# Performance work log

Hardware: AMD Instinct MI355X
Metric: run time of the kernel (lower is better)

The kernel has to match this reference:

```python
import jax, jax.numpy as jnp
import numpy as np

B, T, D = 4096, 64, 250          # batch states, tokens, BiLSTM output size (2*hidden_dim)
S_STACK, S_BUF = 3, 1            # num_stack, num_buffer
H, N_TRANS, N_LABELS = 125, 4, 50


def setup_inputs() -> dict:
    key = jax.random.key(0)
    ks = jax.random.split(key, 16)
    inp = {
        "lstm_out":     jax.random.normal(ks[0], (B, T, D), jnp.float32),
        "stack_index":  jax.random.randint(ks[1], (B, S_STACK), 0, T),
        "stack_len":    jax.random.randint(ks[2], (B,), 0, S_STACK + 1),
        "buffer_index": jax.random.randint(ks[3], (B, S_BUF), 0, T),
        "buffer_len":   jax.random.randint(ks[4], (B,), 0, S_BUF + 1),
        "W1_t": jax.random.normal(ks[5], ((S_STACK + S_BUF) * D, H), jnp.float32) * 0.03,
        "b1_t": jax.random.normal(ks[6], (H,), jnp.float32) * 0.03,
        "W2_t": jax.random.normal(ks[7], (H, N_TRANS), jnp.float32) * 0.03,
        "b2_t": jax.random.normal(ks[8], (N_TRANS,), jnp.float32) * 0.03,
        "W1_r": jax.random.normal(ks[9], ((S_STACK + S_BUF) * D, H), jnp.float32) * 0.03,
        "b1_r": jax.random.normal(ks[10], (H,), jnp.float32) * 0.03,
        "W2_r": jax.random.normal(ks[11], (H, N_LABELS), jnp.float32) * 0.03,
        "b2_r": jax.random.normal(ks[12], (N_LABELS,), jnp.float32) * 0.03,
    }
    return inp


def _gather_pad(lstm_out, index, length):
    # lstm_out: [B, T, D]; index: [B, K]; length: [B]
    # positions >= length[b] receive the zero padding vector (== _mlp_padding)
    g = jnp.take_along_axis(lstm_out, index[:, :, None], axis=1)      # [B, K, D]
    mask = jnp.arange(index.shape[1])[None, :] < length[:, None]      # [B, K]
    g = jnp.where(mask[:, :, None], g, jnp.zeros((), g.dtype))
    return g.reshape(g.shape[0], -1)                                  # [B, K*D]


def _mlp(x, W1, b1, W2, b2):
    # MultilayerPerceptron(input, 125, out) with tanh hidden activation
    h = jnp.tanh(x @ W1 + b1)
    return h @ W2 + b2


def reference(lstm_out, stack_index, stack_len, buffer_index, buffer_len,
              W1_t, b1_t, W2_t, b2_t, W1_r, b1_r, W2_r, b2_r):
    stack_feats = _gather_pad(lstm_out, stack_index, stack_len)    # [B, 3*D]
    buf_feats = _gather_pad(lstm_out, buffer_index, buffer_len)    # [B, 1*D]
    mlp_input = jnp.concatenate([stack_feats, buf_feats], axis=1)  # [B, 4*D]
    # dropout is identity in eval mode
    transitions = jnp.tanh(_mlp(mlp_input, W1_t, b1_t, W2_t, b2_t))
    relations = jnp.tanh(_mlp(mlp_input, W1_r, b1_r, W2_r, b2_r))
    return transitions, relations
```

## Files before the change

### kernel.cpp

```cpp
#include <hip/hip_runtime.h>

#define BATCH 4096
#define TSEQ  64
#define DDIM  250
#define HDIM  125
#define NT    4
#define NL    50
#define KP    1024
#define NP    256

typedef __attribute__((ext_vector_type(8))) __bf16 bf16x8;
typedef __attribute__((ext_vector_type(4))) float  f32x4;

__device__ __forceinline__ unsigned short f32_to_bf16(float f) {
    unsigned int u = __float_as_uint(f);
    u += 0x7FFFu + ((u >> 16) & 1u);
    return (unsigned short)(u >> 16);
}

__global__ __launch_bounds__(256) void prep_kernel(
    const float* __restrict__ lstm_out,
    const int*   __restrict__ stack_index,
    const int*   __restrict__ stack_len,
    const int*   __restrict__ buffer_index,
    const int*   __restrict__ buffer_len,
    const float* __restrict__ W1_t,
    const float* __restrict__ W1_r,
    unsigned short* __restrict__ Xb,
    unsigned short* __restrict__ Wb)
{
    const int blk = blockIdx.x;
    const int t   = threadIdx.x;

    if (blk < BATCH) {
        const int b    = blk;
        const int slen = stack_len[b];
        const int blen = buffer_len[b];
        const int idxB = buffer_index[b];
        const int k0   = t * 4;
        unsigned short v[4];
        #pragma unroll
        for (int i = 0; i < 4; ++i) {
            const int k = k0 + i;
            float f = 0.0f;
            if (k < 1000) {
                const int s = k / 250;
                const int d = k - s * 250;
                const int idxS = stack_index[b * 3 + (s < 3 ? s : 2)];
                const int idx  = (s < 3) ? idxS : idxB;
                const bool valid = (s < 3) ? (s < slen) : (blen > 0);
                if (valid) f = lstm_out[((size_t)b * TSEQ + (size_t)idx) * DDIM + d];
            }
            v[i] = f32_to_bf16(f);
        }
        *reinterpret_cast<ushort4*>(Xb + (size_t)b * KP + k0) =
            make_ushort4(v[0], v[1], v[2], v[3]);
    } else {
        const int n  = blk - BATCH;
        const int k0 = t * 4;
        unsigned short v[4];
        #pragma unroll
        for (int i = 0; i < 4; ++i) {
            const int k = k0 + i;
            float f = 0.0f;
            if (k < 1000 && n < 250) {
                f = (n < HDIM) ? W1_t[(size_t)k * HDIM + n]
                               : W1_r[(size_t)k * HDIM + (n - HDIM)];
            }
            v[i] = f32_to_bf16(f);
        }
        *reinterpret_cast<ushort4*>(Wb + (size_t)n * KP + k0) =
            make_ushort4(v[0], v[1], v[2], v[3]);
    }
}

__global__ __launch_bounds__(256) void gemm_kernel(
    const unsigned short* __restrict__ Xb,
    const unsigned short* __restrict__ Wb,
    const float* __restrict__ b1_t,
    const float* __restrict__ b1_r,
    const float* __restrict__ W2_t,
    const float* __restrict__ b2_t,
    const float* __restrict__ W2_r,
    const float* __restrict__ b2_r,
    float* __restrict__ out_trans,
    float* __restrict__ out_rel)
{
    __shared__ __align__(16) unsigned char XsRaw[16 * 2048];
    __shared__ float h_lds[16][260];

    const int tid = threadIdx.x;
    const int b0  = blockIdx.x * 16;

    #pragma unroll
    for (int i = 0; i < 8; ++i) {
        const int chunk = i * 256 + tid;
        const int row   = chunk >> 7;
        const int c     = chunk & 127;
        uint4 g = *reinterpret_cast<const uint4*>(Xb + (size_t)(b0 + row) * KP + c * 8);
        const int byte = row * 2048 + ((c * 16) ^ ((row & 7) << 4));
        *reinterpret_cast<uint4*>(XsRaw + byte) = g;
    }
    __syncthreads();

    const int lane  = tid & 63;
    const int wave  = tid >> 6;
    const int lrow  = lane & 15;
    const int lk    = (lane >> 4) * 8;
    const int nbase = wave * 64;

    f32x4 acc0 = {0.f,0.f,0.f,0.f}, acc1 = acc0, acc2 = acc0, acc3 = acc0;

    const unsigned short* wbase = Wb + (size_t)(nbase + lrow) * KP + lk;
    const unsigned char*  xrow  = XsRaw + lrow * 2048;
    const int xmask = (lrow & 7) << 4;

    #pragma unroll 8
    for (int ks = 0; ks < 32; ++ks) {
        const int xbyte = ((ks * 32 + lk) * 2) ^ xmask;
        bf16x8 a   = *reinterpret_cast<const bf16x8*>(xrow + xbyte);
        bf16x8 bv0 = *reinterpret_cast<const bf16x8*>(wbase + 0 * 16 * KP + ks * 32);
        bf16x8 bv1 = *reinterpret_cast<const bf16x8*>(wbase + 1 * 16 * KP + ks * 32);
        bf16x8 bv2 = *reinterpret_cast<const bf16x8*>(wbase + 2 * 16 * KP + ks * 32);
        bf16x8 bv3 = *reinterpret_cast<const bf16x8*>(wbase + 3 * 16 * KP + ks * 32);
        acc0 = __builtin_amdgcn_mfma_f32_16x16x32_bf16(a, bv0, acc0, 0, 0, 0);
        acc1 = __builtin_amdgcn_mfma_f32_16x16x32_bf16(a, bv1, acc1, 0, 0, 0);
        acc2 = __builtin_amdgcn_mfma_f32_16x16x32_bf16(a, bv2, acc2, 0, 0, 0);
        acc3 = __builtin_amdgcn_mfma_f32_16x16x32_bf16(a, bv3, acc3, 0, 0, 0);
    }

    {
        const int r0 = (lane >> 4) * 4;
        #pragma unroll
        for (int fn = 0; fn < 4; ++fn) {
            const f32x4 ac = (fn == 0) ? acc0 : (fn == 1) ? acc1 : (fn == 2) ? acc2 : acc3;
            const int col = nbase + fn * 16 + lrow;
            const float bias = (col < HDIM) ? b1_t[col]
                             : (col < 250)  ? b1_r[col - HDIM] : 0.0f;
            #pragma unroll
            for (int rg = 0; rg < 4; ++rg) {
                const float v = tanhf(ac[rg] + bias);
                if (col < HDIM)      h_lds[r0 + rg][col] = v;
                else if (col < 250)  h_lds[r0 + rg][col + 3] = v;
            }
        }
    }
    __syncthreads();

    const int m  = tid & 15;
    const int og = tid >> 4;
    if (og < 14) {
        const bool isT = (og == 0);
        const int  base = isT ? 0 : 128;
        const int  r0   = isT ? 0 : (og - 1) * 4;
        const int  ldw  = isT ? NT : NL;
        const float* __restrict__ W2 = isT ? W2_t : W2_r;
        const float* __restrict__ b2 = isT ? b2_t : b2_r;
        float a0 = 0.f, a1 = 0.f, a2 = 0.f, a3 = 0.f;
        #pragma unroll 4
        for (int k = 0; k < HDIM; ++k) {
            const float h = h_lds[m][base + k];
            const float* w = W2 + (size_t)k * ldw + r0;
            a0 = fmaf(h, w[0], a0);
            if (r0 + 1 < ldw) a1 = fmaf(h, w[1], a1);
            if (r0 + 2 < ldw) a2 = fmaf(h, w[2], a2);
            if (r0 + 3 < ldw) a3 = fmaf(h, w[3], a3);
        }
        float* outp = isT ? (out_trans + (size_t)(b0 + m) * NT)
                          : (out_rel   + (size_t)(b0 + m) * NL);
        if (r0 + 0 < ldw) outp[r0 + 0] = tanhf(a0 + b2[r0 + 0]);
        if (r0 + 1 < ldw) outp[r0 + 1] = tanhf(a1 + b2[r0 + 1]);
        if (r0 + 2 < ldw) outp[r0 + 2] = tanhf(a2 + b2[r0 + 2]);
        if (r0 + 3 < ldw) outp[r0 + 3] = tanhf(a3 + b2[r0 + 3]);
    }
}

extern "C" void kernel_launch(void* const* d_in, const int* in_sizes, int n_in,
                              void* d_out, int out_size, void* d_ws, size_t ws_size,
                              hipStream_t stream) {
    const float* lstm_out     = (const float*)d_in[0];
    const int*   stack_index  = (const int*)  d_in[1];
    const int*   stack_len    = (const int*)  d_in[2];
    const int*   buffer_index = (const int*)  d_in[3];
    const int*   buffer_len   = (const int*)  d_in[4];
    const float* W1_t = (const float*)d_in[5];
    const float* b1_t = (const float*)d_in[6];
    const float* W2_t = (const float*)d_in[7];
    const float* b2_t = (const float*)d_in[8];
    const float* W1_r = (const float*)d_in[9];
    const float* b1_r = (const float*)d_in[10];
    const float* W2_r = (const float*)d_in[11];
    const float* b2_r = (const float*)d_in[12];

    float* out_trans = (float*)d_out;
    float* out_rel   = (float*)d_out + (size_t)BATCH * NT;

    unsigned short* Wb = (unsigned short*)d_ws;
    unsigned short* Xb = Wb + (size_t)NP * KP;

    prep_kernel<<<BATCH + NP, 256, 0, stream>>>(
        lstm_out, stack_index, stack_len, buffer_index, buffer_len,
        W1_t, W1_r, Xb, Wb);

    gemm_kernel<<<BATCH / 16, 256, 0, stream>>>(
        Xb, Wb, b1_t, b1_r, W2_t, b2_t, W2_r, b2_r, out_trans, out_rel);
}
```

Before: 394.8 us.

## Fuse gather into GEMM kernel and pre-swizzle W1 into MFMA fragment layout

Drops the global bf16 X staging buffer: the fused kernel now gathers the stack and buffer rows from lstm_out, converts them to bf16 and writes them straight into swizzled LDS. W1 is prepared by a smaller kernel in MFMA fragment order, so each lane reads its B operand with a contiguous coalesced load. The GEMM block grows to 512 threads, with 8 waves each computing two 16-column tiles. This removes a global round trip of the activations but makes the gather writes to LDS scalar 2-byte stores.

After: 384.8 us. 1.03x faster.

```diff
diff --git a/kernel.cpp b/kernel.cpp
--- a/kernel.cpp
+++ b/kernel.cpp
@@ -7,7 +7,7 @@
 #define NT    4
 #define NL    50
 #define KP    1024
-#define NP    256
+#define KREAL 1000
 
 typedef __attribute__((ext_vector_type(8))) __bf16 bf16x8;
 typedef __attribute__((ext_vector_type(4))) float  f32x4;
@@ -18,65 +18,40 @@
     return (unsigned short)(u >> 16);
 }
 
-__global__ __launch_bounds__(256) void prep_kernel(
+__global__ __launch_bounds__(256) void prep_w_kernel(
+    const float* __restrict__ W1_t,
+    const float* __restrict__ W1_r,
+    unsigned short* __restrict__ Wfrag)
+{
+    const int g    = blockIdx.x * 256 + threadIdx.x;
+    const int f    = g >> 11;
+    const int rem  = g & 2047;
+    const int ks   = rem >> 6;
+    const int lane = rem & 63;
+    const int col  = f * 16 + (lane & 15);
+    const int kb   = ks * 32 + (lane >> 4) * 8;
+    unsigned short v[8];
+    #pragma unroll
+    for (int j = 0; j < 8; ++j) {
+        const int k = kb + j;
+        float x = 0.0f;
+        if (k < KREAL && col < 250) {
+            x = (col < HDIM) ? W1_t[(size_t)k * HDIM + col]
+                             : W1_r[(size_t)k * HDIM + (col - HDIM)];
+        }
+        v[j] = f32_to_bf16(x);
+    }
+    *reinterpret_cast<ushort4*>(Wfrag + (size_t)g * 8)     = make_ushort4(v[0],v[1],v[2],v[3]);
+    *reinterpret_cast<ushort4*>(Wfrag + (size_t)g * 8 + 4) = make_ushort4(v[4],v[5],v[6],v[7]);
+}
+
+__global__ __launch_bounds__(512) void fused_kernel(
     const float* __restrict__ lstm_out,
     const int*   __restrict__ stack_index,
     const int*   __restrict__ stack_len,
     const int*   __restrict__ buffer_index,
     const int*   __restrict__ buffer_len,
-    const float* __restrict__ W1_t,
-    const float* __restrict__ W1_r,
-    unsigned short* __restrict__ Xb,
-    unsigned short* __restrict__ Wb)
-{
-    const int blk = blockIdx.x;
-    const int t   = threadIdx.x;
-
-    if (blk < BATCH) {
-        const int b    = blk;
-        const int slen = stack_len[b];
-        const int blen = buffer_len[b];
-        const int idxB = buffer_index[b];
-        const int k0   = t * 4;
-        unsigned short v[4];
-        #pragma unroll
-        for (int i = 0; i < 4; ++i) {
-            const int k = k0 + i;
-            float f = 0.0f;
-            if (k < 1000) {
-                const int s = k / 250;
-                const int d = k - s * 250;
-                const int idxS = stack_index[b * 3 + (s < 3 ? s : 2)];
-                const int idx  = (s < 3) ? idxS : idxB;
-                const bool valid = (s < 3) ? (s < slen) : (blen > 0);
-                if (valid) f = lstm_out[((size_t)b * TSEQ + (size_t)idx) * DDIM + d];
-            }
-            v[i] = f32_to_bf16(f);
-        }
-        *reinterpret_cast<ushort4*>(Xb + (size_t)b * KP + k0) =
-            make_ushort4(v[0], v[1], v[2], v[3]);
-    } else {
-        const int n  = blk - BATCH;
-        const int k0 = t * 4;
-        unsigned short v[4];
-        #pragma unroll
-        for (int i = 0; i < 4; ++i) {
-            const int k = k0 + i;
-            float f = 0.0f;
-            if (k < 1000 && n < 250) {
-                f = (n < HDIM) ? W1_t[(size_t)k * HDIM + n]
-                               : W1_r[(size_t)k * HDIM + (n - HDIM)];
-            }
-            v[i] = f32_to_bf16(f);
-        }
-        *reinterpret_cast<ushort4*>(Wb + (size_t)n * KP + k0) =
-            make_ushort4(v[0], v[1], v[2], v[3]);
-    }
-}
-
-__global__ __launch_bounds__(256) void gemm_kernel(
-    const unsigned short* __restrict__ Xb,
-    const unsigned short* __restrict__ Wb,
+    const unsigned short* __restrict__ Wfrag,
     const float* __restrict__ b1_t,
     const float* __restrict__ b1_r,
     const float* __restrict__ W2_t,
@@ -86,62 +61,75 @@
     float* __restrict__ out_trans,
     float* __restrict__ out_rel)
 {
-    __shared__ __align__(16) unsigned char XsRaw[16 * 2048];
+    __shared__ __align__(16) unsigned char Xs[16 * 2048];
     __shared__ float h_lds[16][260];
 
-    const int tid = threadIdx.x;
-    const int b0  = blockIdx.x * 16;
+    const int tid  = threadIdx.x;
+    const int wave = tid >> 6;
+    const int lane = tid & 63;
+    const int b0   = blockIdx.x * 16;
 
     #pragma unroll
     for (int i = 0; i < 8; ++i) {
-        const int chunk = i * 256 + tid;
-        const int row   = chunk >> 7;
-        const int c     = chunk & 127;
-        uint4 g = *reinterpret_cast<const uint4*>(Xb + (size_t)(b0 + row) * KP + c * 8);
-        const int byte = row * 2048 + ((c * 16) ^ ((row & 7) << 4));
-        *reinterpret_cast<uint4*>(XsRaw + byte) = g;
+        const int pair = wave * 8 + i;
+        const int m = pair >> 2;
+        const int s = pair & 3;
+        const int b = b0 + m;
+        int idx; bool valid;
+        if (s < 3) { idx = stack_index[b * 3 + s]; valid = (s < stack_len[b]); }
+        else       { idx = buffer_index[b];        valid = (buffer_len[b] > 0); }
+        const float* __restrict__ src = lstm_out + ((size_t)b * TSEQ + (size_t)idx) * DDIM;
+        const int colbase = s * 250;
+        const int xm = (m & 7) << 4;
+        #pragma unroll
+        for (int d0 = 0; d0 < 256; d0 += 64) {
+            const int d = d0 + lane;
+            if (d < 250) {
+                const float x = valid ? src[d] : 0.0f;
+                const int byte = m * 2048 + (((colbase + d) * 2) ^ xm);
+                *reinterpret_cast<unsigned short*>(Xs + byte) = f32_to_bf16(x);
+            }
+        }
+    }
+    if (tid < 384) {
+        const int m = tid / 24;
+        const int c = tid - m * 24;
+        const int byte = m * 2048 + (((1000 + c) * 2) ^ ((m & 7) << 4));
+        *reinterpret_cast<unsigned short*>(Xs + byte) = 0;
     }
     __syncthreads();
 
-    const int lane  = tid & 63;
-    const int wave  = tid >> 6;
     const int lrow  = lane & 15;
     const int lk    = (lane >> 4) * 8;
-    const int nbase = wave * 64;
+    const int xmask = (lrow & 7) << 4;
+    const unsigned char* xrow = Xs + lrow * 2048;
 
-    f32x4 acc0 = {0.f,0.f,0.f,0.f}, acc1 = acc0, acc2 = acc0, acc3 = acc0;
-
-    const unsigned short* wbase = Wb + (size_t)(nbase + lrow) * KP + lk;
-    const unsigned char*  xrow  = XsRaw + lrow * 2048;
-    const int xmask = (lrow & 7) << 4;
+    f32x4 acc0 = {0.f,0.f,0.f,0.f}, acc1 = acc0;
+    const unsigned short* wb0 = Wfrag + ((size_t)(wave * 2 + 0) * 2048 + lane) * 8;
+    const unsigned short* wb1 = Wfrag + ((size_t)(wave * 2 + 1) * 2048 + lane) * 8;
 
     #pragma unroll 8
     for (int ks = 0; ks < 32; ++ks) {
-        const int xbyte = ((ks * 32 + lk) * 2) ^ xmask;
-        bf16x8 a   = *reinterpret_cast<const bf16x8*>(xrow + xbyte);
-        bf16x8 bv0 = *reinterpret_cast<const bf16x8*>(wbase + 0 * 16 * KP + ks * 32);
-        bf16x8 bv1 = *reinterpret_cast<const bf16x8*>(wbase + 1 * 16 * KP + ks * 32);
-        bf16x8 bv2 = *reinterpret_cast<const bf16x8*>(wbase + 2 * 16 * KP + ks * 32);
-        bf16x8 bv3 = *reinterpret_cast<const bf16x8*>(wbase + 3 * 16 * KP + ks * 32);
+        bf16x8 a   = *reinterpret_cast<const bf16x8*>(xrow + (((ks * 32 + lk) * 2) ^ xmask));
+        bf16x8 bv0 = *reinterpret_cast<const bf16x8*>(wb0 + ks * 512);
+        bf16x8 bv1 = *reinterpret_cast<const bf16x8*>(wb1 + ks * 512);
         acc0 = __builtin_amdgcn_mfma_f32_16x16x32_bf16(a, bv0, acc0, 0, 0, 0);
         acc1 = __builtin_amdgcn_mfma_f32_16x16x32_bf16(a, bv1, acc1, 0, 0, 0);
-        acc2 = __builtin_amdgcn_mfma_f32_16x16x32_bf16(a, bv2, acc2, 0, 0, 0);
-        acc3 = __builtin_amdgcn_mfma_f32_16x16x32_bf16(a, bv3, acc3, 0, 0, 0);
     }
 
     {
         const int r0 = (lane >> 4) * 4;
         #pragma unroll
-        for (int fn = 0; fn < 4; ++fn) {
-            const f32x4 ac = (fn == 0) ? acc0 : (fn == 1) ? acc1 : (fn == 2) ? acc2 : acc3;
-            const int col = nbase + fn * 16 + lrow;
+        for (int fn = 0; fn < 2; ++fn) {
+            const f32x4 ac = fn ? acc1 : acc0;
+            const int col = (wave * 2 + fn) * 16 + lrow;
             const float bias = (col < HDIM) ? b1_t[col]
                              : (col < 250)  ? b1_r[col - HDIM] : 0.0f;
             #pragma unroll
             for (int rg = 0; rg < 4; ++rg) {
                 const float v = tanhf(ac[rg] + bias);
-                if (col < HDIM)      h_lds[r0 + rg][col] = v;
-                else if (col < 250)  h_lds[r0 + rg][col + 3] = v;
+                if (col < HDIM)     h_lds[r0 + rg][col] = v;
+                else if (col < 250) h_lds[r0 + rg][col + 3] = v;
             }
         }
     }
@@ -157,7 +145,7 @@
         const float* __restrict__ W2 = isT ? W2_t : W2_r;
         const float* __restrict__ b2 = isT ? b2_t : b2_r;
         float a0 = 0.f, a1 = 0.f, a2 = 0.f, a3 = 0.f;
-        #pragma unroll 4
+        #pragma unroll 5
         for (int k = 0; k < HDIM; ++k) {
             const float h = h_lds[m][base + k];
             const float* w = W2 + (size_t)k * ldw + r0;
@@ -195,13 +183,11 @@
     float* out_trans = (float*)d_out;
     float* out_rel   = (float*)d_out + (size_t)BATCH * NT;
 
-    unsigned short* Wb = (unsigned short*)d_ws;
-    unsigned short* Xb = Wb + (size_t)NP * KP;
+    unsigned short* Wfrag = (unsigned short*)d_ws;
 
-    prep_kernel<<<BATCH + NP, 256, 0, stream>>>(
+    prep_w_kernel<<<128, 256, 0, stream>>>(W1_t, W1_r, Wfrag);
+
+    fused_kernel<<<BATCH / 16, 512, 0, stream>>>(
         lstm_out, stack_index, stack_len, buffer_index, buffer_len,
-        W1_t, W1_r, Xb, Wb);
-
-    gemm_kernel<<<BATCH / 16, 256, 0, stream>>>(
-        Xb, Wb, b1_t, b1_r, W2_t, b2_t, W2_r, b2_r, out_trans, out_rel);
+        Wfrag, b1_t, b1_r, W2_t, b2_t, W2_r, b2_r, out_trans, out_rel);
 }
```
